# Performance work log

Measured on AMD Instinct MI355X. Metric: run time of the kernel, lower is better.

## Reference

```python
import jax, jax.numpy as jnp
import numpy as np

B, S, D, H = 2, 2048, 1024, 16
DK = D // H

def setup_inputs() -> dict:
    key = jax.random.key(0)
    ks = jax.random.split(key, 8)
    inp = {
        "Q": jax.random.normal(ks[0], (B, S, D), dtype=jnp.float32),
        "K": jax.random.normal(ks[1], (B, S, D), dtype=jnp.float32),
        "V": jax.random.normal(ks[2], (B, S, D), dtype=jnp.float32),
        "mask": jax.random.randint(ks[3], (B, 1, S, S), 0, 2, dtype=jnp.int32),
        # nn.Linear weights, shape [out_features, in_features], no bias
        "Wq": jax.random.normal(ks[4], (D, D), dtype=jnp.float32) / np.sqrt(D),
        "Wk": jax.random.normal(ks[5], (D, D), dtype=jnp.float32) / np.sqrt(D),
        "Wv": jax.random.normal(ks[6], (D, D), dtype=jnp.float32) / np.sqrt(D),
        "Wo": jax.random.normal(ks[7], (D, D), dtype=jnp.float32) / np.sqrt(D),
    }
    return inp

def reference(Q, K, V, mask, Wq, Wk, Wv, Wo):
    b, s, d = Q.shape
    # projections: y = x @ W.T (torch nn.Linear convention)
    q = (Q @ Wq.T).reshape(b, s, H, DK).transpose(0, 2, 1, 3)  # [b,h,s,dk]
    k = (K @ Wk.T).reshape(b, -1, H, DK).transpose(0, 2, 1, 3)
    v = (V @ Wv.T).reshape(b, -1, H, DK).transpose(0, 2, 1, 3)
    score = jnp.einsum("bhqd,bhkd->bhqk", q, k) / jnp.sqrt(jnp.float32(DK))
    # faithful to source: masked positions get value 1e-9 BEFORE softmax
    score = jnp.where(mask == 0, jnp.float32(1e-9), score)
    attn = jax.nn.softmax(score, axis=-1)
    # dropout p=0.1 treated as eval-mode identity
    out = jnp.einsum("bhqk,bhkd->bhqd", attn, v)  # [b,h,s,dk]
    out = out.transpose(0, 2, 1, 3).reshape(b, s, d)
    return out @ Wo.T
```

## Files before the change

### kernel.cpp

```cpp
#include <hip/hip_runtime.h>

typedef unsigned short u16;
typedef unsigned char  u8;
typedef unsigned long long u64;
typedef __attribute__((ext_vector_type(8))) short bf16x8;
typedef __attribute__((ext_vector_type(4))) float f32x4;

constexpr int B_  = 2;
constexpr int S_  = 2048;
constexpr int D_  = 1024;
constexpr int H_  = 16;
constexpr int DK_ = 64;
constexpr int NROW = B_ * S_;
constexpr size_t QSZ  = (size_t)B_ * H_ * S_ * DK_;
constexpr size_t XBSZ = (size_t)NROW * D_;
constexpr size_t WBSZ = (size_t)D_ * D_;
constexpr size_t MSZ  = (size_t)B_ * S_ * S_;
constexpr size_t MPKB = MSZ / 8;

__device__ __forceinline__ u16 f2bf(float f) {
    union { float f; unsigned u; } c; c.f = f;
    unsigned r = c.u + 0x7fffu + ((c.u >> 16) & 1u);
    return (u16)(r >> 16);
}
__device__ __forceinline__ unsigned pack2(float a, float b) {
    return (unsigned)f2bf(a) | ((unsigned)f2bf(b) << 16);
}
__device__ __forceinline__ unsigned cvt_pk_bf16(float a, float b) {
    unsigned r;
    asm("v_cvt_pk_bf16_f32 %0, %1, %2" : "=v"(r) : "v"(a), "v"(b));
    return r;
}

__device__ __forceinline__ void gl_lds16(const u16* g, u16* l) {
    __builtin_amdgcn_global_load_lds(
        (const __attribute__((address_space(1))) void*)g,
        (__attribute__((address_space(3))) void*)l, 16, 0, 0);
}

__global__ __launch_bounds__(256)
void cvt7m(const float* __restrict__ s0, const float* __restrict__ s1,
           const float* __restrict__ s2, const float* __restrict__ s3,
           const float* __restrict__ s4, const float* __restrict__ s5,
           const float* __restrict__ s6, const int* __restrict__ mk,
           u16* __restrict__ d0, u16* __restrict__ d1, u16* __restrict__ d2,
           u16* __restrict__ d3, u16* __restrict__ d4, u16* __restrict__ d5,
           u16* __restrict__ d6, u8* __restrict__ mp)
{
    constexpr size_t XT = 3 * XBSZ;
    constexpr int NCF = (int)((3 * XBSZ + 4 * WBSZ) / 2048);
    constexpr int NCM = (int)(MSZ / 2048);

    for (int c = blockIdx.x; c < NCF + NCM; c += gridDim.x) {
        if (c < NCF) {
            const size_t base = (size_t)c * 2048;
            const float* s; u16* d; size_t off;
            if (base < XT) {
                const int a = (int)(base >> 22);
                off = base & (XBSZ - 1);
                s = (a == 0) ? s0 : (a == 1) ? s1 : s2;
                d = (a == 0) ? d0 : (a == 1) ? d1 : d2;
            } else {
                const size_t r = base - XT;
                const int a = (int)(r >> 20);
                off = r & (WBSZ - 1);
                s = (a == 0) ? s3 : (a == 1) ? s4 : (a == 2) ? s5 : s6;
                d = (a == 0) ? d3 : (a == 1) ? d4 : (a == 2) ? d5 : d6;
            }
            const size_t e = off + (size_t)threadIdx.x * 8;
            const float4 x0 = *(const float4*)(s + e);
            const float4 x1 = *(const float4*)(s + e + 4);
            uint4 p;
            p.x = pack2(x0.x, x0.y); p.y = pack2(x0.z, x0.w);
            p.z = pack2(x1.x, x1.y); p.w = pack2(x1.z, x1.w);
            *(uint4*)(d + e) = p;
        } else {
            const size_t e = (size_t)(c - NCF) * 2048 + (size_t)threadIdx.x * 8;
            const int4 x0 = *(const int4*)(mk + e);
            const int4 x1 = *(const int4*)(mk + e + 4);
            unsigned bv = (unsigned)(x0.x != 0)        | ((unsigned)(x0.y != 0) << 1)
                        | ((unsigned)(x0.z != 0) << 2) | ((unsigned)(x0.w != 0) << 3)
                        | ((unsigned)(x1.x != 0) << 4) | ((unsigned)(x1.y != 0) << 5)
                        | ((unsigned)(x1.z != 0) << 6) | ((unsigned)(x1.w != 0) << 7);
            mp[e >> 3] = (u8)bv;
        }
    }
}

__global__ __launch_bounds__(256, 3)
void qkv_gemm(const u16* __restrict__ Xq, const u16* __restrict__ Xk,
              const u16* __restrict__ Xv,
              const u16* __restrict__ Wq, const u16* __restrict__ Wk,
              const u16* __restrict__ Wv,
              u16* __restrict__ Yq, u16* __restrict__ Yk, u16* __restrict__ Yv)
{
    __shared__ u16 As[128 * 32];
    __shared__ u16 Bs[128 * 32];

    const int z = blockIdx.z;
    const u16* X = (z == 0) ? Xq : (z == 1) ? Xk : Xv;
    const u16* W = (z == 0) ? Wq : (z == 1) ? Wk : Wv;
    u16*       Y = (z == 0) ? Yq : (z == 1) ? Yk : Yv;
    const float osc = (z == 0) ? 0.125f : 1.0f;

    const int tid  = threadIdx.x;
    const int lane = tid & 63;
    const int w    = tid >> 6;
    const int quad = lane >> 4;
    const int lq   = lane & 15;
    const int wm   = (w & 1) << 6;
    const int wn   = (w >> 1) << 6;

    const int m0 = blockIdx.x << 7;
    const int n0 = blockIdx.y << 7;

    const int srow = tid >> 2;
    const int scol = (tid & 3) << 3;
    const u16* ga0 = X + (size_t)(m0 + srow) * D_ + scol;
    const u16* ga1 = ga0 + (size_t)64 * D_;
    const u16* gb0 = W + (size_t)(n0 + srow) * D_ + scol;
    const u16* gb1 = gb0 + (size_t)64 * D_;

    u16* la0 = As + (size_t)w * 512;
    u16* la1 = As + 2048 + (size_t)w * 512;
    u16* lb0 = Bs + (size_t)w * 512;
    u16* lb1 = Bs + 2048 + (size_t)w * 512;

    f32x4 acc[4][4];
#pragma unroll
    for (int i = 0; i < 4; ++i)
#pragma unroll
        for (int j = 0; j < 4; ++j) acc[i][j] = (f32x4){0.f, 0.f, 0.f, 0.f};

    for (int kt = 0; kt < D_; kt += 32) {
        __syncthreads();
        gl_lds16(ga0 + kt, la0);
        gl_lds16(ga1 + kt, la1);
        gl_lds16(gb0 + kt, lb0);
        gl_lds16(gb1 + kt, lb1);
        __syncthreads();

        bf16x8 af[4], bf[4];
#pragma unroll
        for (int t = 0; t < 4; ++t) {
            af[t] = *(const bf16x8*)&As[(size_t)(wm + (t << 4) + lq) * 32 + (quad << 3)];
            bf[t] = *(const bf16x8*)&Bs[(size_t)(wn + (t << 4) + lq) * 32 + (quad << 3)];
        }
#pragma unroll
        for (int i = 0; i < 4; ++i)
#pragma unroll
            for (int j = 0; j < 4; ++j)
                acc[i][j] = __builtin_amdgcn_mfma_f32_16x16x32_bf16(
                    af[i], bf[j], acc[i][j], 0, 0, 0);
    }

#pragma unroll
    for (int i = 0; i < 4; ++i)
#pragma unroll
        for (int j = 0; j < 4; ++j)
#pragma unroll
            for (int r = 0; r < 4; ++r) {
                const int grow = m0 + wm + (i << 4) + (quad << 2) + r;
                const int of   = n0 + wn + (j << 4) + lq;
                const int b = grow >> 11, s = grow & (S_ - 1);
                const int h = of >> 6,    dk = of & 63;
                Y[(((size_t)(b * H_ + h)) * S_ + s) * DK_ + dk] =
                    f2bf(acc[i][j][r] * osc);
            }
}

__global__ __launch_bounds__(256, 3)
void out_gemm(const u16* __restrict__ X, const u16* __restrict__ W,
              float* __restrict__ Y)
{
    __shared__ u16 As[128 * 32];
    __shared__ u16 Bs[128 * 32];

    const int tid  = threadIdx.x;
    const int lane = tid & 63;
    const int w    = tid >> 6;
    const int quad = lane >> 4;
    const int lq   = lane & 15;
    const int wm   = (w & 1) << 6;
    const int wn   = (w >> 1) << 6;

    const int m0 = blockIdx.x << 7;
    const int n0 = blockIdx.y << 7;

    const int srow = tid >> 2;
    const int scol = (tid & 3) << 3;
    const u16* ga0 = X + (size_t)(m0 + srow) * D_ + scol;
    const u16* ga1 = ga0 + (size_t)64 * D_;
    const u16* gb0 = W + (size_t)(n0 + srow) * D_ + scol;
    const u16* gb1 = gb0 + (size_t)64 * D_;

    u16* la0 = As + (size_t)w * 512;
    u16* la1 = As + 2048 + (size_t)w * 512;
    u16* lb0 = Bs + (size_t)w * 512;
    u16* lb1 = Bs + 2048 + (size_t)w * 512;

    f32x4 acc[4][4];
#pragma unroll
    for (int i = 0; i < 4; ++i)
#pragma unroll
        for (int j = 0; j < 4; ++j) acc[i][j] = (f32x4){0.f, 0.f, 0.f, 0.f};

    for (int kt = 0; kt < D_; kt += 32) {
        __syncthreads();
        gl_lds16(ga0 + kt, la0);
        gl_lds16(ga1 + kt, la1);
        gl_lds16(gb0 + kt, lb0);
        gl_lds16(gb1 + kt, lb1);
        __syncthreads();

        bf16x8 af[4], bf[4];
#pragma unroll
        for (int t = 0; t < 4; ++t) {
            af[t] = *(const bf16x8*)&As[(size_t)(wm + (t << 4) + lq) * 32 + (quad << 3)];
            bf[t] = *(const bf16x8*)&Bs[(size_t)(wn + (t << 4) + lq) * 32 + (quad << 3)];
        }
#pragma unroll
        for (int i = 0; i < 4; ++i)
#pragma unroll
            for (int j = 0; j < 4; ++j)
                acc[i][j] = __builtin_amdgcn_mfma_f32_16x16x32_bf16(
                    af[i], bf[j], acc[i][j], 0, 0, 0);
    }

#pragma unroll
    for (int i = 0; i < 4; ++i)
#pragma unroll
        for (int j = 0; j < 4; ++j)
#pragma unroll
            for (int r = 0; r < 4; ++r) {
                const int grow = m0 + wm + (i << 4) + (quad << 2) + r;
                const int gcol = n0 + wn + (j << 4) + lq;
                Y[(size_t)grow * D_ + gcol] = acc[i][j][r];
            }
}

constexpr int AP = 72;

__global__ __launch_bounds__(256, 2)
void attn_mfma5(const u16* __restrict__ qb, const u16* __restrict__ kb,
                const u16* __restrict__ vb, const u8* __restrict__ mpk,
                u16* __restrict__ ctx)
{
    __shared__ u16 Qs[128][AP];
    __shared__ u16 Ks[64][AP];
    __shared__ u16 Vt[64][AP];
    __shared__ u16 Ps[128][AP];

    const int tid  = threadIdx.x;
    const int lane = tid & 63;
    const int w    = tid >> 6;
    const int quad = lane >> 4;
    const int lq   = lane & 15;
    const int w32  = w << 5;

    const int q0 = blockIdx.x << 7;
    const int h  = blockIdx.y;
    const int b  = blockIdx.z;

    const u16* qbh = qb + (((size_t)b * H_ + h) * S_ + q0) * DK_;
    const u16* kbh = kb + ((size_t)b * H_ + h) * S_ * DK_;
    const u16* vbh = vb + ((size_t)b * H_ + h) * S_ * DK_;
    const u8*  mbh = mpk + (size_t)b * S_ * (S_ / 8);

    {
        const int r = tid >> 1, c = (tid & 1) << 5;
#pragma unroll
        for (int u = 0; u < 4; ++u)
            *(uint4*)&Qs[r][c + (u << 3)] =
                *(const uint4*)&qbh[(size_t)r * DK_ + c + (u << 3)];
    }
    __syncthreads();
    bf16x8 aQ[2][2];
#pragma unroll
    for (int i = 0; i < 2; ++i) {
        aQ[i][0] = *(const bf16x8*)&Qs[w32 + (i << 4) + lq][quad << 3];
        aQ[i][1] = *(const bf16x8*)&Qs[w32 + (i << 4) + lq][32 + (quad << 3)];
    }

    f32x4 O[2][4];
    float lsum[2][4];
#pragma unroll
    for (int i = 0; i < 2; ++i)
#pragma unroll
        for (int t = 0; t < 4; ++t) O[i][t] = (f32x4){0.f, 0.f, 0.f, 0.f};
#pragma unroll
    for (int i = 0; i < 2; ++i)
#pragma unroll
        for (int r = 0; r < 4; ++r) lsum[i][r] = 0.f;

    const int ksr = tid >> 2, ksc = (tid & 3) << 4;
    const int vkey = lane, vsc = w << 4;
    const int vpc  = ((vkey & 15) << 2) | (vkey >> 4);

    uint4 kr0, kr1; ushort4 vr[4];
    {
        kr0 = *(const uint4*)&kbh[(size_t)ksr * DK_ + ksc];
        kr1 = *(const uint4*)&kbh[(size_t)ksr * DK_ + ksc + 8];
#pragma unroll
        for (int u = 0; u < 4; ++u)
            vr[u] = *(const ushort4*)&vbh[(size_t)vkey * DK_ + vsc + (u << 2)];
    }

    const int qrow0 = q0 + w32 + (quad << 2);
    const u8* mrow = mbh + (size_t)qrow0 * (S_ / 8);

    for (int k0 = 0; k0 < S_; k0 += 64) {
        u64 mw[2][4];
#pragma unroll
        for (int i = 0; i < 2; ++i)
#pragma unroll
            for (int r = 0; r < 4; ++r)
                mw[i][r] = *(const u64*)&mrow[(size_t)((i << 4) + r) * (S_ / 8) + (k0 >> 3)];

        __syncthreads();
        {
            *(uint4*)&Ks[ksr][ksc]     = kr0;
            *(uint4*)&Ks[ksr][ksc + 8] = kr1;
            const u16 vv[16] = {
                vr[0].x, vr[0].y, vr[0].z, vr[0].w,
                vr[1].x, vr[1].y, vr[1].z, vr[1].w,
                vr[2].x, vr[2].y, vr[2].z, vr[2].w,
                vr[3].x, vr[3].y, vr[3].z, vr[3].w };
#pragma unroll
            for (int i = 0; i < 16; ++i)
                Vt[vsc + i][vpc] = vv[i];
        }
        __syncthreads();

        if (k0 + 64 < S_) {
            const size_t kb0 = (size_t)(k0 + 64 + ksr) * DK_ + ksc;
            kr0 = *(const uint4*)&kbh[kb0];
            kr1 = *(const uint4*)&kbh[kb0 + 8];
            const size_t vb0 = (size_t)(k0 + 64 + vkey) * DK_ + vsc;
#pragma unroll
            for (int u = 0; u < 4; ++u)
                vr[u] = *(const ushort4*)&vbh[vb0 + (u << 2)];
        }

        f32x4 st[2][4];
#pragma unroll
        for (int t = 0; t < 4; ++t) {
            const bf16x8 b0 = *(const bf16x8*)&Ks[(t << 4) + lq][quad << 3];
            const bf16x8 b1 = *(const bf16x8*)&Ks[(t << 4) + lq][32 + (quad << 3)];
#pragma unroll
            for (int i = 0; i < 2; ++i) {
                f32x4 c = {0.f, 0.f, 0.f, 0.f};
                c = __builtin_amdgcn_mfma_f32_16x16x32_bf16(aQ[i][0], b0, c, 0, 0, 0);
                c = __builtin_amdgcn_mfma_f32_16x16x32_bf16(aQ[i][1], b1, c, 0, 0, 0);
                st[i][t] = c;
            }
        }

#pragma unroll
        for (int i = 0; i < 2; ++i)
#pragma unroll
            for (int r = 0; r < 4; ++r) {
                const unsigned lo = (unsigned)mw[i][r];
                const unsigned hi = (unsigned)(mw[i][r] >> 32);
                float p0 = __expf(st[i][0][r]);
                float p1 = __expf(st[i][1][r]);
                float p2 = __expf(st[i][2][r]);
                float p3 = __expf(st[i][3][r]);
                p0 = ((lo >> lq) & 1u) ? p0 : 1.0f;
                p1 = ((lo >> (lq + 16)) & 1u) ? p1 : 1.0f;
                p2 = ((hi >> lq) & 1u) ? p2 : 1.0f;
                p3 = ((hi >> (lq + 16)) & 1u) ? p3 : 1.0f;
                lsum[i][r] += (p0 + p1) + (p2 + p3);
                uint2 pw;
                pw.x = cvt_pk_bf16(p0, p1);
                pw.y = cvt_pk_bf16(p2, p3);
                *(uint2*)&Ps[w32 + (i << 4) + (quad << 2) + r][lq << 2] = pw;
            }

        bf16x8 aP[2][2];
#pragma unroll
        for (int i = 0; i < 2; ++i) {
            aP[i][0] = *(const bf16x8*)&Ps[w32 + (i << 4) + lq][quad << 3];
            aP[i][1] = *(const bf16x8*)&Ps[w32 + (i << 4) + lq][32 + (quad << 3)];
        }
#pragma unroll
        for (int t = 0; t < 4; ++t) {
            const bf16x8 b0 = *(const bf16x8*)&Vt[(t << 4) + lq][quad << 3];
            const bf16x8 b1 = *(const bf16x8*)&Vt[(t << 4) + lq][32 + (quad << 3)];
#pragma unroll
            for (int i = 0; i < 2; ++i) {
                O[i][t] = __builtin_amdgcn_mfma_f32_16x16x32_bf16(aP[i][0], b0, O[i][t], 0, 0, 0);
                O[i][t] = __builtin_amdgcn_mfma_f32_16x16x32_bf16(aP[i][1], b1, O[i][t], 0, 0, 0);
            }
        }
    }

#pragma unroll
    for (int i = 0; i < 2; ++i)
#pragma unroll
        for (int r = 0; r < 4; ++r) {
#pragma unroll
            for (int off = 1; off < 16; off <<= 1)
                lsum[i][r] += __shfl_xor(lsum[i][r], off);
            lsum[i][r] = 1.0f / lsum[i][r];
        }

#pragma unroll
    for (int i = 0; i < 2; ++i)
#pragma unroll
        for (int t = 0; t < 4; ++t)
#pragma unroll
            for (int r = 0; r < 4; ++r) {
                const int row = qrow0 + (i << 4) + r;
                ctx[((size_t)b * S_ + row) * D_ + (h << 6) + (t << 4) + lq] =
                    f2bf(O[i][t][r] * lsum[i][r]);
            }
}

extern "C" void kernel_launch(void* const* d_in, const int* in_sizes, int n_in,
                              void* d_out, int out_size, void* d_ws, size_t ws_size,
                              hipStream_t stream)
{
    const float* Q    = (const float*)d_in[0];
    const float* K    = (const float*)d_in[1];
    const float* V    = (const float*)d_in[2];
    const int*   mask = (const int*)d_in[3];
    const float* Wq   = (const float*)d_in[4];
    const float* Wk   = (const float*)d_in[5];
    const float* Wv   = (const float*)d_in[6];
    const float* Wo   = (const float*)d_in[7];
    float* out = (float*)d_out;

    u16* xqb = (u16*)d_ws;
    u16* xkb = xqb + XBSZ;
    u16* xvb = xqb + 2 * XBSZ;
    u16* wqb = xqb + 3 * XBSZ;
    u16* wkb = wqb + WBSZ;
    u16* wvb = wqb + 2 * WBSZ;
    u16* wob = wqb + 3 * WBSZ;
    u16* qw  = wqb + 4 * WBSZ;
    u16* kw  = qw + QSZ;
    u16* vw  = qw + 2 * QSZ;
    u8*  mpk = (u8*)(qw + 3 * QSZ);
    u16* cx  = xqb;

    const dim3 blk(256);

    hipLaunchKernelGGL(cvt7m, dim3(2048), blk, 0, stream,
                       Q, K, V, Wq, Wk, Wv, Wo, mask,
                       xqb, xkb, xvb, wqb, wkb, wvb, wob, mpk);
    hipLaunchKernelGGL(qkv_gemm, dim3(NROW / 128, D_ / 128, 3), blk, 0, stream,
                       xqb, xkb, xvb, wqb, wkb, wvb, qw, kw, vw);
    hipLaunchKernelGGL(attn_mfma5, dim3(S_ / 128, H_, B_), blk, 0, stream,
                       qw, kw, vw, mpk, cx);
    hipLaunchKernelGGL(out_gemm, dim3(NROW / 128, D_ / 128), blk, 0, stream,
                       cx, wob, out);
}
```

Baseline: 254.8 us.

## Widen GEMM k-steps, shrink out-GEMM tiles, swizzle attention blocks, vectorize V transpose

The QKV GEMM now loads two 32-wide K slices per barrier pair, which halves the number of synchronizations per K pass at the cost of double the LDS. The output GEMM moves to 64x64 tiles with 64-wide K steps and a higher occupancy hint, giving a grid four times larger for better CU fill. The attention kernel remaps block IDs with a swizzle so that blocks running at the same time touch different heads or batches. Its V transpose into LDS now uses 16-byte global loads and paired 32-bit shared-memory stores in place of scattered 16-bit writes. Smaller output tiles lower data reuse per block, and the swizzle may change cache locality.

```diff
diff --git a/kernel.cpp b/kernel.cpp
--- a/kernel.cpp
+++ b/kernel.cpp
@@ -94,8 +94,8 @@
               const u16* __restrict__ Wv,
               u16* __restrict__ Yq, u16* __restrict__ Yk, u16* __restrict__ Yv)
 {
-    __shared__ u16 As[128 * 32];
-    __shared__ u16 Bs[128 * 32];
+    __shared__ u16 As[2 * 128 * 32];
+    __shared__ u16 Bs[2 * 128 * 32];
 
     const int z = blockIdx.z;
     const u16* X = (z == 0) ? Xq : (z == 1) ? Xk : Xv;
@@ -132,26 +132,33 @@
 #pragma unroll
         for (int j = 0; j < 4; ++j) acc[i][j] = (f32x4){0.f, 0.f, 0.f, 0.f};
 
-    for (int kt = 0; kt < D_; kt += 32) {
+    for (int kt = 0; kt < D_; kt += 64) {
         __syncthreads();
         gl_lds16(ga0 + kt, la0);
         gl_lds16(ga1 + kt, la1);
         gl_lds16(gb0 + kt, lb0);
         gl_lds16(gb1 + kt, lb1);
-        __syncthreads();
-
-        bf16x8 af[4], bf[4];
-#pragma unroll
-        for (int t = 0; t < 4; ++t) {
-            af[t] = *(const bf16x8*)&As[(size_t)(wm + (t << 4) + lq) * 32 + (quad << 3)];
-            bf[t] = *(const bf16x8*)&Bs[(size_t)(wn + (t << 4) + lq) * 32 + (quad << 3)];
-        }
-#pragma unroll
-        for (int i = 0; i < 4; ++i)
-#pragma unroll
-            for (int j = 0; j < 4; ++j)
-                acc[i][j] = __builtin_amdgcn_mfma_f32_16x16x32_bf16(
-                    af[i], bf[j], acc[i][j], 0, 0, 0);
+        gl_lds16(ga0 + kt + 32, la0 + 4096);
+        gl_lds16(ga1 + kt + 32, la1 + 4096);
+        gl_lds16(gb0 + kt + 32, lb0 + 4096);
+        gl_lds16(gb1 + kt + 32, lb1 + 4096);
+        __syncthreads();
+
+#pragma unroll
+        for (int kk = 0; kk < 2; ++kk) {
+            bf16x8 af[4], bf[4];
+#pragma unroll
+            for (int t = 0; t < 4; ++t) {
+                af[t] = *(const bf16x8*)&As[(kk << 12) + (size_t)(wm + (t << 4) + lq) * 32 + (quad << 3)];
+                bf[t] = *(const bf16x8*)&Bs[(kk << 12) + (size_t)(wn + (t << 4) + lq) * 32 + (quad << 3)];
+            }
+#pragma unroll
+            for (int i = 0; i < 4; ++i)
+#pragma unroll
+                for (int j = 0; j < 4; ++j)
+                    acc[i][j] = __builtin_amdgcn_mfma_f32_16x16x32_bf16(
+                        af[i], bf[j], acc[i][j], 0, 0, 0);
+        }
     }
 
 #pragma unroll
@@ -169,68 +176,67 @@
             }
 }
 
-__global__ __launch_bounds__(256, 3)
+__global__ __launch_bounds__(256, 4)
 void out_gemm(const u16* __restrict__ X, const u16* __restrict__ W,
               float* __restrict__ Y)
 {
-    __shared__ u16 As[128 * 32];
-    __shared__ u16 Bs[128 * 32];
+    __shared__ u16 As[2 * 64 * 32];
+    __shared__ u16 Bs[2 * 64 * 32];
 
     const int tid  = threadIdx.x;
     const int lane = tid & 63;
     const int w    = tid >> 6;
     const int quad = lane >> 4;
     const int lq   = lane & 15;
-    const int wm   = (w & 1) << 6;
-    const int wn   = (w >> 1) << 6;
-
-    const int m0 = blockIdx.x << 7;
-    const int n0 = blockIdx.y << 7;
+    const int wm   = (w & 1) << 5;
+    const int wn   = (w >> 1) << 5;
+
+    const int m0 = blockIdx.x << 6;
+    const int n0 = blockIdx.y << 6;
 
     const int srow = tid >> 2;
     const int scol = (tid & 3) << 3;
     const u16* ga0 = X + (size_t)(m0 + srow) * D_ + scol;
-    const u16* ga1 = ga0 + (size_t)64 * D_;
     const u16* gb0 = W + (size_t)(n0 + srow) * D_ + scol;
-    const u16* gb1 = gb0 + (size_t)64 * D_;
 
     u16* la0 = As + (size_t)w * 512;
-    u16* la1 = As + 2048 + (size_t)w * 512;
     u16* lb0 = Bs + (size_t)w * 512;
-    u16* lb1 = Bs + 2048 + (size_t)w * 512;
-
-    f32x4 acc[4][4];
-#pragma unroll
-    for (int i = 0; i < 4; ++i)
-#pragma unroll
-        for (int j = 0; j < 4; ++j) acc[i][j] = (f32x4){0.f, 0.f, 0.f, 0.f};
-
-    for (int kt = 0; kt < D_; kt += 32) {
+
+    f32x4 acc[2][2];
+#pragma unroll
+    for (int i = 0; i < 2; ++i)
+#pragma unroll
+        for (int j = 0; j < 2; ++j) acc[i][j] = (f32x4){0.f, 0.f, 0.f, 0.f};
+
+    for (int kt = 0; kt < D_; kt += 64) {
         __syncthreads();
         gl_lds16(ga0 + kt, la0);
-        gl_lds16(ga1 + kt, la1);
         gl_lds16(gb0 + kt, lb0);
-        gl_lds16(gb1 + kt, lb1);
-        __syncthreads();
-
-        bf16x8 af[4], bf[4];
-#pragma unroll
-        for (int t = 0; t < 4; ++t) {
-            af[t] = *(const bf16x8*)&As[(size_t)(wm + (t << 4) + lq) * 32 + (quad << 3)];
-            bf[t] = *(const bf16x8*)&Bs[(size_t)(wn + (t << 4) + lq) * 32 + (quad << 3)];
-        }
-#pragma unroll
-        for (int i = 0; i < 4; ++i)
-#pragma unroll
-            for (int j = 0; j < 4; ++j)
-                acc[i][j] = __builtin_amdgcn_mfma_f32_16x16x32_bf16(
-                    af[i], bf[j], acc[i][j], 0, 0, 0);
-    }
-
-#pragma unroll
-    for (int i = 0; i < 4; ++i)
-#pragma unroll
-        for (int j = 0; j < 4; ++j)
+        gl_lds16(ga0 + kt + 32, la0 + 2048);
+        gl_lds16(gb0 + kt + 32, lb0 + 2048);
+        __syncthreads();
+
+#pragma unroll
+        for (int kk = 0; kk < 2; ++kk) {
+            bf16x8 af[2], bf[2];
+#pragma unroll
+            for (int t = 0; t < 2; ++t) {
+                af[t] = *(const bf16x8*)&As[(kk << 11) + (size_t)(wm + (t << 4) + lq) * 32 + (quad << 3)];
+                bf[t] = *(const bf16x8*)&Bs[(kk << 11) + (size_t)(wn + (t << 4) + lq) * 32 + (quad << 3)];
+            }
+#pragma unroll
+            for (int i = 0; i < 2; ++i)
+#pragma unroll
+                for (int j = 0; j < 2; ++j)
+                    acc[i][j] = __builtin_amdgcn_mfma_f32_16x16x32_bf16(
+                        af[i], bf[j], acc[i][j], 0, 0, 0);
+        }
+    }
+
+#pragma unroll
+    for (int i = 0; i < 2; ++i)
+#pragma unroll
+        for (int j = 0; j < 2; ++j)
 #pragma unroll
             for (int r = 0; r < 4; ++r) {
                 const int grow = m0 + wm + (i << 4) + (quad << 2) + r;
@@ -242,7 +248,7 @@
 constexpr int AP = 72;
 
 __global__ __launch_bounds__(256, 2)
-void attn_mfma5(const u16* __restrict__ qb, const u16* __restrict__ kb,
+void attn_mfma8(const u16* __restrict__ qb, const u16* __restrict__ kb,
                 const u16* __restrict__ vb, const u8* __restrict__ mpk,
                 u16* __restrict__ ctx)
 {
@@ -258,14 +264,15 @@
     const int lq   = lane & 15;
     const int w32  = w << 5;
 
-    const int q0 = blockIdx.x << 7;
-    const int h  = blockIdx.y;
-    const int b  = blockIdx.z;
+    const int bid = (int)(blockIdx.x + gridDim.x * (blockIdx.y + gridDim.y * blockIdx.z));
+    const int swz = (bid & 7) * 64 + (bid >> 3);
+    const int q0 = (swz & 15) << 7;
+    const int h  = (swz >> 4) & 15;
+    const int b  = swz >> 8;
 
     const u16* qbh = qb + (((size_t)b * H_ + h) * S_ + q0) * DK_;
     const u16* kbh = kb + ((size_t)b * H_ + h) * S_ * DK_;
     const u16* vbh = vb + ((size_t)b * H_ + h) * S_ * DK_;
-    const u8*  mbh = mpk + (size_t)b * S_ * (S_ / 8);
 
     {
         const int r = tid >> 1, c = (tid & 1) << 5;
@@ -294,20 +301,22 @@
         for (int r = 0; r < 4; ++r) lsum[i][r] = 0.f;
 
     const int ksr = tid >> 2, ksc = (tid & 3) << 4;
-    const int vkey = lane, vsc = w << 4;
-    const int vpc  = ((vkey & 15) << 2) | (vkey >> 4);
-
-    uint4 kr0, kr1; ushort4 vr[4];
+    const int vc  = tid & 15;
+    const int vs  = (tid >> 4) & 1;
+    const int vk0 = vc + (vs << 5);
+    const int vdg = tid >> 5;
+    const int vcol = (vc << 2) + (vs << 1);
+
+    uint4 kr0, kr1, vr0, vr1;
     {
         kr0 = *(const uint4*)&kbh[(size_t)ksr * DK_ + ksc];
         kr1 = *(const uint4*)&kbh[(size_t)ksr * DK_ + ksc + 8];
-#pragma unroll
-        for (int u = 0; u < 4; ++u)
-            vr[u] = *(const ushort4*)&vbh[(size_t)vkey * DK_ + vsc + (u << 2)];
+        vr0 = *(const uint4*)&vbh[(size_t)vk0 * DK_ + (vdg << 3)];
+        vr1 = *(const uint4*)&vbh[(size_t)(vk0 + 16) * DK_ + (vdg << 3)];
     }
 
     const int qrow0 = q0 + w32 + (quad << 2);
-    const u8* mrow = mbh + (size_t)qrow0 * (S_ / 8);
+    const u8* mrow = mpk + (size_t)b * S_ * (S_ / 8) + (size_t)qrow0 * (S_ / 8);
 
     for (int k0 = 0; k0 < S_; k0 += 64) {
         u64 mw[2][4];
@@ -321,14 +330,11 @@
         {
             *(uint4*)&Ks[ksr][ksc]     = kr0;
             *(uint4*)&Ks[ksr][ksc + 8] = kr1;
-            const u16 vv[16] = {
-                vr[0].x, vr[0].y, vr[0].z, vr[0].w,
-                vr[1].x, vr[1].y, vr[1].z, vr[1].w,
-                vr[2].x, vr[2].y, vr[2].z, vr[2].w,
-                vr[3].x, vr[3].y, vr[3].z, vr[3].w };
-#pragma unroll
-            for (int i = 0; i < 16; ++i)
-                Vt[vsc + i][vpc] = vv[i];
+            const u16* a0 = (const u16*)&vr0;
+            const u16* a1 = (const u16*)&vr1;
+#pragma unroll
+            for (int i = 0; i < 8; ++i)
+                *(ushort2*)&Vt[(vdg << 3) + i][vcol] = (ushort2){a0[i], a1[i]};
         }
         __syncthreads();
 
@@ -336,10 +342,9 @@
             const size_t kb0 = (size_t)(k0 + 64 + ksr) * DK_ + ksc;
             kr0 = *(const uint4*)&kbh[kb0];
             kr1 = *(const uint4*)&kbh[kb0 + 8];
-            const size_t vb0 = (size_t)(k0 + 64 + vkey) * DK_ + vsc;
-#pragma unroll
-            for (int u = 0; u < 4; ++u)
-                vr[u] = *(const ushort4*)&vbh[vb0 + (u << 2)];
+            const size_t vb0 = (size_t)(k0 + 64 + vk0) * DK_ + (vdg << 3);
+            vr0 = *(const uint4*)&vbh[vb0];
+            vr1 = *(const uint4*)&vbh[vb0 + (size_t)16 * DK_];
         }
 
         f32x4 st[2][4];
@@ -444,15 +449,13 @@
     u8*  mpk = (u8*)(qw + 3 * QSZ);
     u16* cx  = xqb;
 
-    const dim3 blk(256);
-
-    hipLaunchKernelGGL(cvt7m, dim3(2048), blk, 0, stream,
+    hipLaunchKernelGGL(cvt7m, dim3(2048), dim3(256), 0, stream,
                        Q, K, V, Wq, Wk, Wv, Wo, mask,
                        xqb, xkb, xvb, wqb, wkb, wvb, wob, mpk);
-    hipLaunchKernelGGL(qkv_gemm, dim3(NROW / 128, D_ / 128, 3), blk, 0, stream,
+    hipLaunchKernelGGL(qkv_gemm, dim3(NROW / 128, D_ / 128, 3), dim3(256), 0, stream,
                        xqb, xkb, xvb, wqb, wkb, wvb, qw, kw, vw);
-    hipLaunchKernelGGL(attn_mfma5, dim3(S_ / 128, H_, B_), blk, 0, stream,
+    hipLaunchKernelGGL(attn_mfma8, dim3(S_ / 128, H_, B_), dim3(256), 0, stream,
                        qw, kw, vw, mpk, cx);
-    hipLaunchKernelGGL(out_gemm, dim3(NROW / 128, D_ / 128), blk, 0, stream,
+    hipLaunchKernelGGL(out_gemm, dim3(NROW / 64, D_ / 64), dim3(256), 0, stream,
                        cx, wob, out);
 }
```

Measured after the change: 252.0 us. No clear change (-1.1%).
